# Performance work log

Hardware: AMD Instinct MI355X
Metric: run time of the kernel (lower is better)

## Reference

```python
import jax, jax.numpy as jnp
import numpy as np

DIM_K = 128
MODEL_DIM = 1024
B, S = 8, 2048

def setup_inputs() -> dict:
    key = jax.random.key(0)
    k1, k2, k3, k4, k5, k6, k7 = jax.random.split(key, 7)
    return {
        "query": jax.random.normal(k1, (B, S, MODEL_DIM), dtype=jnp.float32),
        "key": jax.random.normal(k2, (B, S, MODEL_DIM), dtype=jnp.float32),
        "value": jax.random.normal(k3, (B, S, MODEL_DIM), dtype=jnp.float32),
        "mask": jax.random.randint(k4, (B, S, S), 0, 2, dtype=jnp.int32),
        # nn.Linear(model_dim, dim_k, bias=False): weight shape [dim_k, model_dim]
        "Wq": jax.random.normal(k5, (DIM_K, MODEL_DIM), dtype=jnp.float32) * (MODEL_DIM ** -0.5),
        "Wk": jax.random.normal(k6, (DIM_K, MODEL_DIM), dtype=jnp.float32) * (MODEL_DIM ** -0.5),
        "Wv": jax.random.normal(k7, (DIM_K, MODEL_DIM), dtype=jnp.float32) * (MODEL_DIM ** -0.5),
    }

def reference(query, key, value, mask, Wq, Wk, Wv):
    # projections: y = x @ W.T
    q = jnp.einsum('bsm,km->bsk', query, Wq)
    k = jnp.einsum('bsm,km->bsk', key, Wk)
    v = jnp.einsum('bsm,km->bsk', value, Wv)
    scale = 1.0 / jnp.sqrt(jnp.float32(DIM_K))
    pre_score = jnp.einsum('bqk,bsk->bqs', q, k) * scale  # [B,Sq,Sk]
    pre_score = jnp.where(mask == 0, jnp.float32(-1e9), pre_score)
    score = jax.nn.softmax(pre_score, axis=-1)
    return jnp.einsum('bqs,bsk->bqk', score, v)
```

## Files before the change

kernel.cpp:

```cpp
#include <hip/hip_runtime.h>
#include <hip/hip_bf16.h>

#define SEQ 2048
#define DMODEL 1024
#define DK 128

typedef __bf16 bf16x8 __attribute__((ext_vector_type(8)));
typedef float  f32x4  __attribute__((ext_vector_type(4)));

#define L2E 1.44269504088896340736f

#define WS_Q  786432
#define WS_K  2883584
#define WS_VT 4980736
#define WS_BF16_BYTES 14155776ull

__global__ __launch_bounds__(256) void wconv_kernel(
    const float* __restrict__ wq, const float* __restrict__ wk,
    const float* __restrict__ wv, __bf16* __restrict__ wpack)
{
    int i = blockIdx.x * 256 + threadIdx.x;
    int p = i >> 17;
    int j = i & 131071;
    const float* src = (p == 0) ? wq : ((p == 1) ? wk : wv);
    float f = src[j];
    if (p == 0) f *= 0.08838834764831845f;
    __bf16 h = (__bf16)f;
    __bf16 l = (__bf16)(f - (float)h);
    wpack[p * 262144 + j]          = h;
    wpack[p * 262144 + 131072 + j] = l;
}

__global__ __launch_bounds__(256) void proj_kernel(
    const float* __restrict__ xq, const float* __restrict__ xk,
    const float* __restrict__ xv, const __bf16* __restrict__ wpack,
    __bf16* __restrict__ qws, __bf16* __restrict__ kws, __bf16* __restrict__ vtws)
{
    const int p = blockIdx.y;
    const float* __restrict__ x = (p == 0) ? xq : ((p == 1) ? xk : xv);
    const __bf16* __restrict__ whi_g = wpack + p * 262144;
    const __bf16* __restrict__ wlo_g = whi_g + 131072;

    const int mtile = blockIdx.x;
    const int m0 = mtile << 6;
    const int t = threadIdx.x;
    const int wv_ = t >> 6;
    const int lane = t & 63;
    const int l15 = lane & 15, g = lane >> 4;

    __shared__ __align__(16) __bf16 smem[18432];
    __bf16* whl = smem;
    __bf16* wll = smem + 9216;

    f32x4 acc[8];
#pragma unroll
    for (int nt = 0; nt < 8; ++nt) acc[nt] = (f32x4){0.f, 0.f, 0.f, 0.f};

    for (int kk = 0; kk < 16; ++kk) {
        __syncthreads();
#pragma unroll
        for (int i = 0; i < 8; ++i) {
            int idx = i * 256 + t;
            int h = idx >> 10, rem = idx & 1023;
            int row = rem >> 3, ck = rem & 7;
            const __bf16* src = (h ? wlo_g : whi_g) + row * 1024 + kk * 64 + ck * 8;
            __bf16* dst = (h ? wll : whl) + row * 72 + ck * 8;
            *(bf16x8*)dst = *(const bf16x8*)src;
        }
        __syncthreads();

#pragma unroll
        for (int ks = 0; ks < 2; ++ks) {
            int row = m0 + wv_ * 16 + l15;
            int col = kk * 64 + ks * 32 + g * 8;
            const float* xp = x + (size_t)row * 1024 + col;
            f32x4 a0 = *(const f32x4*)xp;
            f32x4 a1 = *(const f32x4*)(xp + 4);
            bf16x8 ah;
#pragma unroll
            for (int j = 0; j < 4; ++j) {
                ah[j] = (__bf16)a0[j];
                ah[4 + j] = (__bf16)a1[j];
            }
#pragma unroll
            for (int nt = 0; nt < 8; ++nt) {
                const __bf16* bp = whl + (nt * 16 + l15) * 72 + ks * 32 + g * 8;
                bf16x8 bh = *(const bf16x8*)bp;
                bf16x8 bl = *(const bf16x8*)(bp + 9216);
                acc[nt] = __builtin_amdgcn_mfma_f32_16x16x32_bf16(ah, bh, acc[nt], 0, 0, 0);
                acc[nt] = __builtin_amdgcn_mfma_f32_16x16x32_bf16(ah, bl, acc[nt], 0, 0, 0);
            }
        }
    }

    __syncthreads();
    __bf16* olds = smem;
#pragma unroll
    for (int nt = 0; nt < 8; ++nt)
#pragma unroll
        for (int r = 0; r < 4; ++r) {
            int rowl = wv_ * 16 + g * 4 + r;
            int col = nt * 16 + l15;
            __bf16 v = (__bf16)acc[nt][r];
            if (p < 2) olds[rowl * 136 + col] = v;
            else       olds[col * 72 + rowl] = v;
        }
    __syncthreads();

    const int bq = mtile >> 5, s0 = (mtile & 31) << 6;
    if (p < 2) {
#pragma unroll
        for (int i = 0; i < 4; ++i) {
            int idx = i * 256 + t;
            int row = idx >> 4, ck = idx & 15;
            bf16x8 v = *(const bf16x8*)(olds + row * 136 + ck * 8);
            __bf16* dst = ((p == 0) ? qws : kws) + (size_t)(m0 + row) * 128 + ck * 8;
            *(bf16x8*)dst = v;
        }
    } else {
#pragma unroll
        for (int i = 0; i < 4; ++i) {
            int idx = i * 256 + t;
            int row = idx >> 3, ck = idx & 7;
            bf16x8 v = *(const bf16x8*)(olds + row * 72 + ck * 8);
            __bf16* dst = vtws + ((size_t)(bq * 128 + row)) * 2048 + s0 + ck * 8;
            *(bf16x8*)dst = v;
        }
    }
}

__global__ __launch_bounds__(256) void flash_kernel(
    const __bf16* __restrict__ qws, const __bf16* __restrict__ kws,
    const __bf16* __restrict__ vtws, const int* __restrict__ mask,
    float* __restrict__ out, float* __restrict__ part, float* __restrict__ mlbuf,
    int ktp)
{
    const int bb = blockIdx.x & 7;
    const int rest = blockIdx.x >> 3;
    const int mtile = rest & 31;
    const int jsplit = rest >> 5;
    const int sq0 = mtile << 6;
    const int t = threadIdx.x;
    const int wv_ = t >> 6;
    const int lane = t & 63;
    const int l15 = lane & 15, g = lane >> 4;

    __shared__ __align__(16) __bf16 smem[22528];
    __bf16* klds = smem;
    __bf16* vtlds = smem + 8704;
    __bf16* plds = smem + 17920 + wv_ * 1152;

    bf16x8 qf[4];
    {
        const __bf16* qp = qws + ((size_t)(bb * 2048 + sq0 + wv_ * 16 + l15)) * 128 + g * 8;
#pragma unroll
        for (int ks = 0; ks < 4; ++ks) qf[ks] = *(const bf16x8*)(qp + ks * 32);
    }

    f32x4 o[8];
#pragma unroll
    for (int nt = 0; nt < 8; ++nt) o[nt] = (f32x4){0.f, 0.f, 0.f, 0.f};
    float m_run[4], l_run[4];
#pragma unroll
    for (int r = 0; r < 4; ++r) { m_run[r] = -__builtin_inff(); l_run[r] = 0.f; }

    const int* mbase = mask + ((size_t)(bb * 2048 + sq0 + wv_ * 16 + g * 4)) * 2048 + l15;

    const int kt_begin = jsplit * ktp, kt_end = kt_begin + ktp;
    for (int kt = kt_begin; kt < kt_end; ++kt) {
        const int n0 = kt << 6;
        __syncthreads();
#pragma unroll
        for (int i = 0; i < 8; ++i) {
            int idx = i * 256 + t;
            if (idx < 1024) {
                int row = idx >> 4, ck = idx & 15;
                *(bf16x8*)(klds + row * 136 + ck * 8) =
                    *(const bf16x8*)(kws + ((size_t)(bb * 2048 + n0 + row)) * 128 + ck * 8);
            } else {
                int v = idx - 1024;
                int row = v >> 3, ck = v & 7;
                *(bf16x8*)(vtlds + row * 72 + ck * 8) =
                    *(const bf16x8*)(vtws + ((size_t)(bb * 128 + row)) * 2048 + n0 + ck * 8);
            }
        }
        __syncthreads();

        int mv[4][4];
#pragma unroll
        for (int nt = 0; nt < 4; ++nt)
#pragma unroll
            for (int r = 0; r < 4; ++r)
                mv[nt][r] = mbase[(size_t)r * 2048 + n0 + nt * 16];

        f32x4 sf[4];
#pragma unroll
        for (int nt = 0; nt < 4; ++nt) sf[nt] = (f32x4){0.f, 0.f, 0.f, 0.f};
#pragma unroll
        for (int nt = 0; nt < 4; ++nt) {
            const __bf16* kp = klds + (nt * 16 + l15) * 136 + g * 8;
#pragma unroll
            for (int ks = 0; ks < 4; ++ks) {
                bf16x8 bfk = *(const bf16x8*)(kp + ks * 32);
                sf[nt] = __builtin_amdgcn_mfma_f32_16x16x32_bf16(qf[ks], bfk, sf[nt], 0, 0, 0);
            }
        }

        float mx[4], mnew[4], alpha[4], psum[4];
#pragma unroll
        for (int r = 0; r < 4; ++r)
            mx[r] = fmaxf(fmaxf(sf[0][r], sf[1][r]), fmaxf(sf[2][r], sf[3][r]));
#pragma unroll
        for (int off = 1; off < 16; off <<= 1)
#pragma unroll
            for (int r = 0; r < 4; ++r)
                mx[r] = fmaxf(mx[r], __shfl_xor(mx[r], off, 64));
#pragma unroll
        for (int r = 0; r < 4; ++r) {
            mnew[r] = fmaxf(m_run[r], mx[r]);
            alpha[r] = exp2f((m_run[r] - mnew[r]) * L2E);
            psum[r] = 0.f;
        }
#pragma unroll
        for (int nt = 0; nt < 4; ++nt)
#pragma unroll
            for (int r = 0; r < 4; ++r) {
                float pv = exp2f((sf[nt][r] - mnew[r]) * L2E);
                pv = mv[nt][r] ? pv : 0.f;
                psum[r] += pv;
                plds[(g * 4 + r) * 72 + nt * 16 + l15] = (__bf16)pv;
            }
#pragma unroll
        for (int off = 1; off < 16; off <<= 1)
#pragma unroll
            for (int r = 0; r < 4; ++r)
                psum[r] += __shfl_xor(psum[r], off, 64);
#pragma unroll
        for (int r = 0; r < 4; ++r) {
            l_run[r] = l_run[r] * alpha[r] + psum[r];
            m_run[r] = mnew[r];
        }
#pragma unroll
        for (int nt = 0; nt < 8; ++nt)
#pragma unroll
            for (int r = 0; r < 4; ++r) o[nt][r] *= alpha[r];

        bf16x8 pa[2];
#pragma unroll
        for (int ks2 = 0; ks2 < 2; ++ks2)
            pa[ks2] = *(const bf16x8*)(plds + l15 * 72 + ks2 * 32 + g * 8);

#pragma unroll
        for (int nt2 = 0; nt2 < 8; ++nt2) {
            const __bf16* vp = vtlds + (nt2 * 16 + l15) * 72 + g * 8;
#pragma unroll
            for (int ks2 = 0; ks2 < 2; ++ks2) {
                bf16x8 bfv = *(const bf16x8*)(vp + ks2 * 32);
                o[nt2] = __builtin_amdgcn_mfma_f32_16x16x32_bf16(pa[ks2], bfv, o[nt2], 0, 0, 0);
            }
        }
    }

    if (part == nullptr) {
        float inv[4];
#pragma unroll
        for (int r = 0; r < 4; ++r) inv[r] = 1.0f / l_run[r];
#pragma unroll
        for (int nt2 = 0; nt2 < 8; ++nt2)
#pragma unroll
            for (int r = 0; r < 4; ++r)
                out[((size_t)(bb * 2048 + sq0 + wv_ * 16 + g * 4 + r)) * 128 + nt2 * 16 + l15] =
                    o[nt2][r] * inv[r];
    } else {
#pragma unroll
        for (int nt2 = 0; nt2 < 8; ++nt2)
#pragma unroll
            for (int r = 0; r < 4; ++r) {
                size_t rowg = (size_t)(bb * 2048 + sq0 + wv_ * 16 + g * 4 + r);
                part[((size_t)jsplit * 16384 + rowg) * 128 + nt2 * 16 + l15] = o[nt2][r];
            }
        if (l15 == 0) {
#pragma unroll
            for (int r = 0; r < 4; ++r) {
                size_t rowg = (size_t)(bb * 2048 + sq0 + wv_ * 16 + g * 4 + r);
                mlbuf[((size_t)jsplit * 16384 + rowg) * 2]     = m_run[r];
                mlbuf[((size_t)jsplit * 16384 + rowg) * 2 + 1] = l_run[r];
            }
        }
    }
}

__global__ __launch_bounds__(256) void merge_kernel(
    const float* __restrict__ part, const float* __restrict__ mlbuf,
    float* __restrict__ out, int J)
{
    int t = threadIdx.x;
    size_t row = (size_t)blockIdx.x * 8 + (t >> 5);
    int c = (t & 31) * 4;
    float mj[4];
    float m = -__builtin_inff();
    for (int j = 0; j < J; ++j) {
        mj[j] = mlbuf[((size_t)j * 16384 + row) * 2];
        m = fmaxf(m, mj[j]);
    }
    float l = 0.f;
    f32x4 acc = (f32x4){0.f, 0.f, 0.f, 0.f};
    for (int j = 0; j < J; ++j) {
        float w = exp2f((mj[j] - m) * L2E);
        l += w * mlbuf[((size_t)j * 16384 + row) * 2 + 1];
        f32x4 v = *(const f32x4*)(part + ((size_t)j * 16384 + row) * 128 + c);
#pragma unroll
        for (int e = 0; e < 4; ++e) acc[e] += w * v[e];
    }
    float inv = 1.0f / l;
#pragma unroll
    for (int e = 0; e < 4; ++e) acc[e] *= inv;
    *(f32x4*)(out + row * 128 + c) = acc;
}

extern "C" void kernel_launch(void* const* d_in, const int* in_sizes, int n_in,
                              void* d_out, int out_size, void* d_ws, size_t ws_size,
                              hipStream_t stream)
{
    const float* query = (const float*)d_in[0];
    const float* key   = (const float*)d_in[1];
    const float* value = (const float*)d_in[2];
    const int*   mask  = (const int*)d_in[3];
    const float* Wq    = (const float*)d_in[4];
    const float* Wk    = (const float*)d_in[5];
    const float* Wv    = (const float*)d_in[6];
    float* out = (float*)d_out;

    __bf16* wpack = (__bf16*)d_ws;
    __bf16* qws = wpack + WS_Q;
    __bf16* kws = wpack + WS_K;
    __bf16* vtws = wpack + WS_VT;

    const size_t per_split = 16384ull * 128 * 4 + 16384ull * 8;
    int J = 1;
    if (ws_size >= WS_BF16_BYTES + 4 * per_split)      J = 4;
    else if (ws_size >= WS_BF16_BYTES + 2 * per_split) J = 2;
    float* part = (J > 1) ? (float*)((char*)d_ws + WS_BF16_BYTES) : nullptr;
    float* mlbuf = (J > 1) ? (part + (size_t)J * 16384 * 128) : nullptr;

    wconv_kernel<<<1536, 256, 0, stream>>>(Wq, Wk, Wv, wpack);
    proj_kernel<<<dim3(256, 3), 256, 0, stream>>>(query, key, value, wpack, qws, kws, vtws);
    flash_kernel<<<256 * J, 256, 0, stream>>>(qws, kws, vtws, mask, out, part, mlbuf, 32 / J);
    if (J > 1) merge_kernel<<<2048, 256, 0, stream>>>(part, mlbuf, out, J);
}
```

Measured before the change: 414.3 us.

## Pre-pack weights and K/V in MFMA fragment order, drop LDS staging

The weight conversion kernel now writes Wq/Wk/Wv in MFMA fragment order. The projection kernel then reads B fragments straight from global memory, with no LDS staging or barriers, and software-prefetches the next x slice. The projection also emits K and V in per-tile fragment-packed layouts, so the flash kernel loads K/V operands directly from global/L2 instead of cooperatively staging them in LDS each tile. The log2(e) factor is folded into the Q weight scale to remove a multiply per exp. Launch-bound occupancy hints are added. The trade-off is that redundant global loads across the four waves now depend on L2/L1 hits, in place of shared LDS reuse.

```diff
diff --git a/kernel.cpp b/kernel.cpp
--- a/kernel.cpp
+++ b/kernel.cpp
@@ -1,18 +1,12 @@
 #include <hip/hip_runtime.h>
 #include <hip/hip_bf16.h>
 
-#define SEQ 2048
-#define DMODEL 1024
-#define DK 128
-
 typedef __bf16 bf16x8 __attribute__((ext_vector_type(8)));
 typedef float  f32x4  __attribute__((ext_vector_type(4)));
 
-#define L2E 1.44269504088896340736f
-
 #define WS_Q  786432
-#define WS_K  2883584
-#define WS_VT 4980736
+#define WS_KP 2883584
+#define WS_VP 4980736
 #define WS_BF16_BYTES 14155776ull
 
 __global__ __launch_bounds__(256) void wconv_kernel(
@@ -20,26 +14,28 @@
     const float* __restrict__ wv, __bf16* __restrict__ wpack)
 {
     int i = blockIdx.x * 256 + threadIdx.x;
-    int p = i >> 17;
-    int j = i & 131071;
+    int p = i >> 17, o = i & 131071;
+    int c = o >> 3, j = o & 7;
+    int l15 = c & 15, g = (c >> 4) & 3, nt = (c >> 6) & 7, ks = (c >> 9) & 1, kk = c >> 10;
+    int col = nt * 16 + l15;
+    int k = kk * 64 + ks * 32 + g * 8 + j;
     const float* src = (p == 0) ? wq : ((p == 1) ? wk : wv);
-    float f = src[j];
-    if (p == 0) f *= 0.08838834764831845f;
+    float f = src[col * 1024 + k];
+    if (p == 0) f *= (0.08838834764831845f * 1.44269504088896340736f);
     __bf16 h = (__bf16)f;
     __bf16 l = (__bf16)(f - (float)h);
-    wpack[p * 262144 + j]          = h;
-    wpack[p * 262144 + 131072 + j] = l;
-}
-
-__global__ __launch_bounds__(256) void proj_kernel(
+    wpack[p * 262144 + o]          = h;
+    wpack[p * 262144 + 131072 + o] = l;
+}
+
+__global__ __launch_bounds__(256, 4) void proj_kernel(
     const float* __restrict__ xq, const float* __restrict__ xk,
     const float* __restrict__ xv, const __bf16* __restrict__ wpack,
-    __bf16* __restrict__ qws, __bf16* __restrict__ kws, __bf16* __restrict__ vtws)
+    __bf16* __restrict__ qws, __bf16* __restrict__ kpack, __bf16* __restrict__ vpack)
 {
     const int p = blockIdx.y;
     const float* __restrict__ x = (p == 0) ? xq : ((p == 1) ? xk : xv);
-    const __bf16* __restrict__ whi_g = wpack + p * 262144;
-    const __bf16* __restrict__ wlo_g = whi_g + 131072;
+    const __bf16* __restrict__ wf = wpack + p * 262144;
 
     const int mtile = blockIdx.x;
     const int m0 = mtile << 6;
@@ -48,53 +44,49 @@
     const int lane = t & 63;
     const int l15 = lane & 15, g = lane >> 4;
 
-    __shared__ __align__(16) __bf16 smem[18432];
-    __bf16* whl = smem;
-    __bf16* wll = smem + 9216;
+    __shared__ __align__(16) __bf16 olds[9216];
 
     f32x4 acc[8];
 #pragma unroll
     for (int nt = 0; nt < 8; ++nt) acc[nt] = (f32x4){0.f, 0.f, 0.f, 0.f};
 
+    const float* xrow = x + (size_t)(m0 + wv_ * 16 + l15) * 1024 + g * 8;
+
+    f32x4 a0 = *(const f32x4*)(xrow);
+    f32x4 a1 = *(const f32x4*)(xrow + 4);
+    f32x4 b0 = *(const f32x4*)(xrow + 32);
+    f32x4 b1 = *(const f32x4*)(xrow + 36);
+
     for (int kk = 0; kk < 16; ++kk) {
-        __syncthreads();
-#pragma unroll
-        for (int i = 0; i < 8; ++i) {
-            int idx = i * 256 + t;
-            int h = idx >> 10, rem = idx & 1023;
-            int row = rem >> 3, ck = rem & 7;
-            const __bf16* src = (h ? wlo_g : whi_g) + row * 1024 + kk * 64 + ck * 8;
-            __bf16* dst = (h ? wll : whl) + row * 72 + ck * 8;
-            *(bf16x8*)dst = *(const bf16x8*)src;
-        }
-        __syncthreads();
-
-#pragma unroll
-        for (int ks = 0; ks < 2; ++ks) {
-            int row = m0 + wv_ * 16 + l15;
-            int col = kk * 64 + ks * 32 + g * 8;
-            const float* xp = x + (size_t)row * 1024 + col;
-            f32x4 a0 = *(const f32x4*)xp;
-            f32x4 a1 = *(const f32x4*)(xp + 4);
-            bf16x8 ah;
-#pragma unroll
-            for (int j = 0; j < 4; ++j) {
-                ah[j] = (__bf16)a0[j];
-                ah[4 + j] = (__bf16)a1[j];
-            }
-#pragma unroll
-            for (int nt = 0; nt < 8; ++nt) {
-                const __bf16* bp = whl + (nt * 16 + l15) * 72 + ks * 32 + g * 8;
-                bf16x8 bh = *(const bf16x8*)bp;
-                bf16x8 bl = *(const bf16x8*)(bp + 9216);
-                acc[nt] = __builtin_amdgcn_mfma_f32_16x16x32_bf16(ah, bh, acc[nt], 0, 0, 0);
-                acc[nt] = __builtin_amdgcn_mfma_f32_16x16x32_bf16(ah, bl, acc[nt], 0, 0, 0);
-            }
-        }
-    }
-
-    __syncthreads();
-    __bf16* olds = smem;
+        f32x4 na0, na1, nb0, nb1;
+        if (kk < 15) {
+            const float* nx = xrow + (kk + 1) * 64;
+            na0 = *(const f32x4*)(nx);
+            na1 = *(const f32x4*)(nx + 4);
+            nb0 = *(const f32x4*)(nx + 32);
+            nb1 = *(const f32x4*)(nx + 36);
+        }
+        bf16x8 ah0, ah1;
+#pragma unroll
+        for (int j = 0; j < 4; ++j) {
+            ah0[j] = (__bf16)a0[j]; ah0[4 + j] = (__bf16)a1[j];
+            ah1[j] = (__bf16)b0[j]; ah1[4 + j] = (__bf16)b1[j];
+        }
+        const __bf16* wb = wf + kk * 8192 + lane * 8;
+#pragma unroll
+        for (int nt = 0; nt < 8; ++nt) {
+            bf16x8 bh0 = *(const bf16x8*)(wb + nt * 512);
+            bf16x8 bl0 = *(const bf16x8*)(wb + nt * 512 + 131072);
+            bf16x8 bh1 = *(const bf16x8*)(wb + nt * 512 + 4096);
+            bf16x8 bl1 = *(const bf16x8*)(wb + nt * 512 + 4096 + 131072);
+            acc[nt] = __builtin_amdgcn_mfma_f32_16x16x32_bf16(ah0, bh0, acc[nt], 0, 0, 0);
+            acc[nt] = __builtin_amdgcn_mfma_f32_16x16x32_bf16(ah0, bl0, acc[nt], 0, 0, 0);
+            acc[nt] = __builtin_amdgcn_mfma_f32_16x16x32_bf16(ah1, bh1, acc[nt], 0, 0, 0);
+            acc[nt] = __builtin_amdgcn_mfma_f32_16x16x32_bf16(ah1, bl1, acc[nt], 0, 0, 0);
+        }
+        a0 = na0; a1 = na1; b0 = nb0; b1 = nb1;
+    }
+
 #pragma unroll
     for (int nt = 0; nt < 8; ++nt)
 #pragma unroll
@@ -107,31 +99,38 @@
         }
     __syncthreads();
 
-    const int bq = mtile >> 5, s0 = (mtile & 31) << 6;
-    if (p < 2) {
+    if (p == 0) {
 #pragma unroll
         for (int i = 0; i < 4; ++i) {
             int idx = i * 256 + t;
             int row = idx >> 4, ck = idx & 15;
             bf16x8 v = *(const bf16x8*)(olds + row * 136 + ck * 8);
-            __bf16* dst = ((p == 0) ? qws : kws) + (size_t)(m0 + row) * 128 + ck * 8;
-            *(bf16x8*)dst = v;
-        }
-    } else {
+            *(bf16x8*)(qws + (size_t)(m0 + row) * 128 + ck * 8) = v;
+        }
+    } else if (p == 1) {
 #pragma unroll
         for (int i = 0; i < 4; ++i) {
             int idx = i * 256 + t;
-            int row = idx >> 3, ck = idx & 7;
-            bf16x8 v = *(const bf16x8*)(olds + row * 72 + ck * 8);
-            __bf16* dst = vtws + ((size_t)(bq * 128 + row)) * 2048 + s0 + ck * 8;
-            *(bf16x8*)dst = v;
-        }
-    }
-}
-
-__global__ __launch_bounds__(256) void flash_kernel(
-    const __bf16* __restrict__ qws, const __bf16* __restrict__ kws,
-    const __bf16* __restrict__ vtws, const int* __restrict__ mask,
+            int ks = idx >> 8, nt = (idx >> 6) & 3, ln = idx & 63;
+            int gg = ln >> 4, ll = ln & 15;
+            bf16x8 v = *(const bf16x8*)(olds + (nt * 16 + ll) * 136 + ks * 32 + gg * 8);
+            *(bf16x8*)(kpack + ((size_t)mtile * 1024 + idx) * 8) = v;
+        }
+    } else {
+#pragma unroll
+        for (int i = 0; i < 4; ++i) {
+            int idx = i * 256 + t;
+            int ks2 = idx >> 9, nt2 = (idx >> 6) & 7, ln = idx & 63;
+            int gg = ln >> 4, ll = ln & 15;
+            bf16x8 v = *(const bf16x8*)(olds + (nt2 * 16 + ll) * 72 + ks2 * 32 + gg * 8);
+            *(bf16x8*)(vpack + ((size_t)mtile * 1024 + idx) * 8) = v;
+        }
+    }
+}
+
+__global__ __launch_bounds__(256, 3) void flash_kernel(
+    const __bf16* __restrict__ qws, const __bf16* __restrict__ kpack,
+    const __bf16* __restrict__ vpack, const int* __restrict__ mask,
     float* __restrict__ out, float* __restrict__ part, float* __restrict__ mlbuf,
     int ktp)
 {
@@ -145,10 +144,8 @@
     const int lane = t & 63;
     const int l15 = lane & 15, g = lane >> 4;
 
-    __shared__ __align__(16) __bf16 smem[22528];
-    __bf16* klds = smem;
-    __bf16* vtlds = smem + 8704;
-    __bf16* plds = smem + 17920 + wv_ * 1152;
+    __shared__ __align__(16) __bf16 psmem[4 * 1152];
+    __bf16* plds = psmem + wv_ * 1152;
 
     bf16x8 qf[4];
     {
@@ -165,26 +162,12 @@
     for (int r = 0; r < 4; ++r) { m_run[r] = -__builtin_inff(); l_run[r] = 0.f; }
 
     const int* mbase = mask + ((size_t)(bb * 2048 + sq0 + wv_ * 16 + g * 4)) * 2048 + l15;
+    const __bf16* kbase = kpack + ((size_t)(bb * 32) * 1024) * 8 + lane * 8;
+    const __bf16* vbase = vpack + ((size_t)(bb * 32) * 1024) * 8 + lane * 8;
 
     const int kt_begin = jsplit * ktp, kt_end = kt_begin + ktp;
     for (int kt = kt_begin; kt < kt_end; ++kt) {
         const int n0 = kt << 6;
-        __syncthreads();
-#pragma unroll
-        for (int i = 0; i < 8; ++i) {
-            int idx = i * 256 + t;
-            if (idx < 1024) {
-                int row = idx >> 4, ck = idx & 15;
-                *(bf16x8*)(klds + row * 136 + ck * 8) =
-                    *(const bf16x8*)(kws + ((size_t)(bb * 2048 + n0 + row)) * 128 + ck * 8);
-            } else {
-                int v = idx - 1024;
-                int row = v >> 3, ck = v & 7;
-                *(bf16x8*)(vtlds + row * 72 + ck * 8) =
-                    *(const bf16x8*)(vtws + ((size_t)(bb * 128 + row)) * 2048 + n0 + ck * 8);
-            }
-        }
-        __syncthreads();
 
         int mv[4][4];
 #pragma unroll
@@ -193,18 +176,17 @@
             for (int r = 0; r < 4; ++r)
                 mv[nt][r] = mbase[(size_t)r * 2048 + n0 + nt * 16];
 
+        const __bf16* kb = kbase + kt * 8192;
         f32x4 sf[4];
 #pragma unroll
         for (int nt = 0; nt < 4; ++nt) sf[nt] = (f32x4){0.f, 0.f, 0.f, 0.f};
 #pragma unroll
-        for (int nt = 0; nt < 4; ++nt) {
-            const __bf16* kp = klds + (nt * 16 + l15) * 136 + g * 8;
+        for (int nt = 0; nt < 4; ++nt)
 #pragma unroll
             for (int ks = 0; ks < 4; ++ks) {
-                bf16x8 bfk = *(const bf16x8*)(kp + ks * 32);
+                bf16x8 bfk = *(const bf16x8*)(kb + (ks * 4 + nt) * 512);
                 sf[nt] = __builtin_amdgcn_mfma_f32_16x16x32_bf16(qf[ks], bfk, sf[nt], 0, 0, 0);
             }
-        }
 
         float mx[4], mnew[4], alpha[4], psum[4];
 #pragma unroll
@@ -218,14 +200,14 @@
 #pragma unroll
         for (int r = 0; r < 4; ++r) {
             mnew[r] = fmaxf(m_run[r], mx[r]);
-            alpha[r] = exp2f((m_run[r] - mnew[r]) * L2E);
+            alpha[r] = exp2f(m_run[r] - mnew[r]);
             psum[r] = 0.f;
         }
 #pragma unroll
         for (int nt = 0; nt < 4; ++nt)
 #pragma unroll
             for (int r = 0; r < 4; ++r) {
-                float pv = exp2f((sf[nt][r] - mnew[r]) * L2E);
+                float pv = exp2f(sf[nt][r] - mnew[r]);
                 pv = mv[nt][r] ? pv : 0.f;
                 psum[r] += pv;
                 plds[(g * 4 + r) * 72 + nt * 16 + l15] = (__bf16)pv;
@@ -250,15 +232,14 @@
         for (int ks2 = 0; ks2 < 2; ++ks2)
             pa[ks2] = *(const bf16x8*)(plds + l15 * 72 + ks2 * 32 + g * 8);
 
-#pragma unroll
-        for (int nt2 = 0; nt2 < 8; ++nt2) {
-            const __bf16* vp = vtlds + (nt2 * 16 + l15) * 72 + g * 8;
+        const __bf16* vb = vbase + kt * 8192;
+#pragma unroll
+        for (int nt2 = 0; nt2 < 8; ++nt2)
 #pragma unroll
             for (int ks2 = 0; ks2 < 2; ++ks2) {
-                bf16x8 bfv = *(const bf16x8*)(vp + ks2 * 32);
+                bf16x8 bfv = *(const bf16x8*)(vb + (ks2 * 8 + nt2) * 512);
                 o[nt2] = __builtin_amdgcn_mfma_f32_16x16x32_bf16(pa[ks2], bfv, o[nt2], 0, 0, 0);
             }
-        }
     }
 
     if (part == nullptr) {
@@ -306,7 +287,7 @@
     float l = 0.f;
     f32x4 acc = (f32x4){0.f, 0.f, 0.f, 0.f};
     for (int j = 0; j < J; ++j) {
-        float w = exp2f((mj[j] - m) * L2E);
+        float w = exp2f(mj[j] - m);
         l += w * mlbuf[((size_t)j * 16384 + row) * 2 + 1];
         f32x4 v = *(const f32x4*)(part + ((size_t)j * 16384 + row) * 128 + c);
 #pragma unroll
@@ -333,8 +314,8 @@
 
     __bf16* wpack = (__bf16*)d_ws;
     __bf16* qws = wpack + WS_Q;
-    __bf16* kws = wpack + WS_K;
-    __bf16* vtws = wpack + WS_VT;
+    __bf16* kpack = wpack + WS_KP;
+    __bf16* vpack = wpack + WS_VP;
 
     const size_t per_split = 16384ull * 128 * 4 + 16384ull * 8;
     int J = 1;
@@ -344,7 +325,7 @@
     float* mlbuf = (J > 1) ? (part + (size_t)J * 16384 * 128) : nullptr;
 
     wconv_kernel<<<1536, 256, 0, stream>>>(Wq, Wk, Wv, wpack);
-    proj_kernel<<<dim3(256, 3), 256, 0, stream>>>(query, key, value, wpack, qws, kws, vtws);
-    flash_kernel<<<256 * J, 256, 0, stream>>>(qws, kws, vtws, mask, out, part, mlbuf, 32 / J);
+    proj_kernel<<<dim3(256, 3), 256, 0, stream>>>(query, key, value, wpack, qws, kpack, vpack);
+    flash_kernel<<<256 * J, 256, 0, stream>>>(qws, kpack, vpack, mask, out, part, mlbuf, 32 / J);
     if (J > 1) merge_kernel<<<2048, 256, 0, stream>>>(part, mlbuf, out, J);
 }
```

Result: slower. 434.1 us (+4.8%).
